# Performance work log

Hardware: AMD Instinct MI355X
Metric: run time of the kernel (lower is better)

The kernel has to match this reference:

```python
import jax, jax.numpy as jnp
import numpy as np

B, S, D, H = 4, 2048, 1024, 16
HD = D // H


def setup_inputs() -> dict:
    key = jax.random.key(0)
    ks = jax.random.split(key, 12)
    sc = 1.0 / np.sqrt(D)
    return {
        "x": jax.random.normal(ks[0], (B, S, D), dtype=jnp.float32),
        "key_padding_mask": jax.random.randint(ks[1], (B, S), 0, 2).astype(bool),
        "attn_mask_modifier": jax.random.uniform(ks[2], (B, S, S), dtype=jnp.float32),
        "Wq": jax.random.normal(ks[3], (D, D), dtype=jnp.float32) * sc,
        "bq": jax.random.normal(ks[4], (D,), dtype=jnp.float32) * sc,
        "Wk": jax.random.normal(ks[5], (D, D), dtype=jnp.float32) * sc,
        "bk": jax.random.normal(ks[6], (D,), dtype=jnp.float32) * sc,
        "Wv": jax.random.normal(ks[7], (D, D), dtype=jnp.float32) * sc,
        "bv": jax.random.normal(ks[8], (D,), dtype=jnp.float32) * sc,
        "Wo": jax.random.normal(ks[9], (D, D), dtype=jnp.float32) * sc,
        "bo": jax.random.normal(ks[10], (D,), dtype=jnp.float32) * sc,
    }


def reference(x, key_padding_mask, attn_mask_modifier, Wq, bq, Wk, bk, Wv, bv, Wo, bo):
    b, s, d = x.shape
    hd = d // H
    # QKV projections -> [b, H, s, hd]
    q = (x @ Wq + bq).reshape(b, s, H, hd).transpose(0, 2, 1, 3)
    k = (x @ Wk + bk).reshape(b, s, H, hd).transpose(0, 2, 1, 3)
    v = (x @ Wv + bv).reshape(b, s, H, hd).transpose(0, 2, 1, 3)
    energy = jnp.einsum("bhqd,bhkd->bhqk", q, k) / jnp.sqrt(jnp.asarray(hd, x.dtype))
    # handle_neg=False path: multiplicative mask modifier, broadcast over heads
    energy = energy * attn_mask_modifier[:, None, :, :]
    # key_padding_mask is applied on the QUERY axis (unsqueeze(1).unsqueeze(-1)) per source
    energy = jnp.where(key_padding_mask[:, None, :, None], jnp.asarray(-1e10, x.dtype), energy)
    attn = jax.nn.softmax(energy, axis=-1)
    out = jnp.einsum("bhqk,bhkd->bhqd", attn, v).transpose(0, 2, 1, 3).reshape(b, s, d)
    return out @ Wo + bo
```

## Files before the change

### kernel.cpp

```cpp
#include <hip/hip_runtime.h>
#include <cstddef>

constexpr int Bn  = 4;
constexpr int Sn  = 2048;
constexpr int Dn  = 1024;
constexpr int Hn  = 16;
constexpr int HDn = 64;

typedef __bf16 bf16;
typedef __attribute__((ext_vector_type(8))) __bf16 bf16x8;
typedef __attribute__((ext_vector_type(4))) __bf16 bf16x4;
typedef __attribute__((ext_vector_type(4))) float  f32x4;

typedef __attribute__((address_space(1))) const void gvoid;
typedef __attribute__((address_space(3))) void lvoid;

__global__ __launch_bounds__(256) void conv_f32_bf16_k(
    const float* __restrict__ in, bf16* __restrict__ out, int n)
{
    int i = (blockIdx.x * 256 + threadIdx.x) * 4;
    if (i + 3 < n) {
        float4 v = *(const float4*)(in + i);
        bf16 o[4] = {(bf16)v.x, (bf16)v.y, (bf16)v.z, (bf16)v.w};
        *(ulong1*)(out + i) = *(ulong1*)o;
    }
}

__global__ __launch_bounds__(256) void bias_cat_k(
    const float* __restrict__ bq, const float* __restrict__ bk,
    const float* __restrict__ bv, float* __restrict__ o)
{
    const int i = blockIdx.x * 256 + threadIdx.x;
    if (i < 1024)      o[i] = bq[i];
    else if (i < 2048) o[i] = bk[i - 1024];
    else if (i < 3072) o[i] = bv[i - 2048];
}

__global__ __launch_bounds__(256) void conv_wt_k(
    const float* __restrict__ w0, const float* __restrict__ w1,
    const float* __restrict__ w2, const float* __restrict__ w3,
    bf16* __restrict__ o0, bf16* __restrict__ o1,
    bf16* __restrict__ o2, bf16* __restrict__ o3)
{
    const float* W = (blockIdx.z == 0) ? w0 : (blockIdx.z == 1) ? w1
                   : (blockIdx.z == 2) ? w2 : w3;
    bf16* O = (blockIdx.z == 0) ? o0 : (blockIdx.z == 1) ? o1
            : (blockIdx.z == 2) ? o2 : o3;
    __shared__ float t[64][65];
    const int tid = threadIdx.x;
    const int k0 = blockIdx.x * 64;
    const int n0 = blockIdx.y * 64;
    #pragma unroll
    for (int p = 0; p < 16; ++p) {
        const int idx = p * 256 + tid;
        const int r = idx >> 6, c = idx & 63;
        t[r][c] = W[(size_t)(k0 + r) * Dn + n0 + c];
    }
    __syncthreads();
    #pragma unroll
    for (int p = 0; p < 16; ++p) {
        const int idx = p * 256 + tid;
        const int r = idx >> 6, c = idx & 63;
        O[(size_t)(n0 + r) * Dn + k0 + c] = (bf16)t[c][r];
    }
}

#define GEMM_STAGE(Ap, Bp, k0, boff)                                          \
    {                                                                         \
        _Pragma("unroll")                                                     \
        for (int j = 0; j < 4; ++j) {                                         \
            const int rbase = (w * 4 + j) * 8;                                \
            const int r = rbase + srow;                                       \
            __builtin_amdgcn_global_load_lds(                                 \
                (gvoid*)(Ap + (size_t)(m0 + r) * Dn + (k0) + scol),           \
                (lvoid*)&smem[(boff) + rbase * 64], 16, 0, 0);                \
            __builtin_amdgcn_global_load_lds(                                 \
                (gvoid*)(Bp + (size_t)(n0 + r) * Dn + (k0) + scol),           \
                (lvoid*)&smem[(boff) + 128 * 64 + rbase * 64], 16, 0, 0);     \
        }                                                                     \
    }

#define GEMM_COMPUTE(boff)                                                    \
    {                                                                         \
        _Pragma("unroll")                                                     \
        for (int ks = 0; ks < 64; ks += 32) {                                 \
            bf16x8 af[4], bfr[4];                                             \
            _Pragma("unroll")                                                 \
            for (int fm = 0; fm < 4; ++fm)                                    \
                af[fm] = *(const bf16x8*)&smem[(boff) +                       \
                    (wm * 64 + fm * 16 + l15) * 64 + ks + quad * 8];          \
            _Pragma("unroll")                                                 \
            for (int fn = 0; fn < 4; ++fn)                                    \
                bfr[fn] = *(const bf16x8*)&smem[(boff) + 128 * 64 +           \
                    (wn * 64 + fn * 16 + l15) * 64 + ks + quad * 8];          \
            _Pragma("unroll")                                                 \
            for (int fm = 0; fm < 4; ++fm)                                    \
                _Pragma("unroll")                                             \
                for (int fn = 0; fn < 4; ++fn)                                \
                    acc[fm][fn] = __builtin_amdgcn_mfma_f32_16x16x32_bf16(    \
                        af[fm], bfr[fn], acc[fm][fn], 0, 0, 0);               \
        }                                                                     \
    }

constexpr int BUF = 2 * 128 * 64;

__global__ __launch_bounds__(256) void gemm_out_k(
    const bf16* __restrict__ A, const bf16* __restrict__ Bt,
    const float* __restrict__ bias, float* __restrict__ outv)
{
    __shared__ __align__(16) bf16 smem[2 * BUF];

    const int tid  = threadIdx.x;
    const int w    = tid >> 6;
    const int lane = tid & 63;
    const int quad = lane >> 4;
    const int l15  = lane & 15;
    const int m0   = blockIdx.x * 128;
    const int n0   = blockIdx.y * 128;
    const int wm   = w >> 1;
    const int wn   = w & 1;
    const int srow = lane >> 3;
    const int scol = (lane & 7) * 8;

    f32x4 acc[4][4] = {};

    GEMM_STAGE(A, Bt, 0, 0);
    __syncthreads();

    int boff = 0;
    for (int kt = 0; kt < Dn / 64; ++kt) {
        if (kt + 1 < Dn / 64) GEMM_STAGE(A, Bt, (kt + 1) * 64, boff ^ BUF);
        GEMM_COMPUTE(boff);
        __syncthreads();
        boff ^= BUF;
    }

    #pragma unroll
    for (int fn = 0; fn < 4; ++fn) {
        const int c = n0 + wn * 64 + fn * 16 + l15;
        const float bv = bias[c];
        #pragma unroll
        for (int fm = 0; fm < 4; ++fm)
            #pragma unroll
            for (int i = 0; i < 4; ++i) {
                const int m = m0 + wm * 64 + fm * 16 + quad * 4 + i;
                outv[(size_t)m * Dn + c] = acc[fm][fn][i] + bv;
            }
    }
}

__global__ __launch_bounds__(256) void gemm_qkv_k(
    const bf16* __restrict__ A, const bf16* __restrict__ Wt,
    const float* __restrict__ bias, bf16* __restrict__ qout,
    bf16* __restrict__ kout, bf16* __restrict__ vout, float scq)
{
    __shared__ __align__(16) bf16 smem[2 * BUF];

    const int tid  = threadIdx.x;
    const int w    = tid >> 6;
    const int lane = tid & 63;
    const int quad = lane >> 4;
    const int l15  = lane & 15;
    const int m0   = blockIdx.x * 128;
    const int n0   = blockIdx.y * 128;
    const int wm   = w >> 1;
    const int wn   = w & 1;
    const int srow = lane >> 3;
    const int scol = (lane & 7) * 8;

    f32x4 acc[4][4] = {};

    GEMM_STAGE(A, Wt, 0, 0);
    __syncthreads();

    int boff = 0;
    for (int kt = 0; kt < Dn / 64; ++kt) {
        if (kt + 1 < Dn / 64) GEMM_STAGE(A, Wt, (kt + 1) * 64, boff ^ BUF);
        GEMM_COMPUTE(boff);
        __syncthreads();
        boff ^= BUF;
    }

    const int sec = n0 >> 10;
    const int cb  = n0 & 1023;

    if (sec < 2) {
        bf16* const outp = sec ? kout : qout;
        const float scale = sec ? 1.0f : scq;
        #pragma unroll
        for (int fn = 0; fn < 4; ++fn) {
            const int cc = cb + wn * 64 + fn * 16 + l15;
            const float bv = bias[n0 + wn * 64 + fn * 16 + l15];
            const int h = cc >> 6, hd = cc & 63;
            #pragma unroll
            for (int fm = 0; fm < 4; ++fm)
                #pragma unroll
                for (int i = 0; i < 4; ++i) {
                    const int m = m0 + wm * 64 + fm * 16 + quad * 4 + i;
                    const int b = m >> 11, s = m & (Sn - 1);
                    outp[(((size_t)(b * Hn + h) * Sn) + s) * HDn + hd] =
                        (bf16)((acc[fm][fn][i] + bv) * scale);
                }
        }
    } else {
        bf16* const T = smem;
        #pragma unroll
        for (int fn = 0; fn < 4; ++fn) {
            const int n = wn * 64 + fn * 16 + l15;
            const float bv = bias[n0 + n];
            #pragma unroll
            for (int fm = 0; fm < 4; ++fm) {
                const int m = wm * 64 + fm * 16 + quad * 4;
                bf16x4 pk;
                #pragma unroll
                for (int i = 0; i < 4; ++i)
                    pk[i] = (bf16)(acc[fm][fn][i] + bv);
                *(bf16x4*)&T[n * 136 + m] = pk;
            }
        }
        __syncthreads();
        const int b  = m0 >> 11;
        const int s0 = m0 & (Sn - 1);
        #pragma unroll
        for (int it = 0; it < 8; ++it) {
            const int n    = it * 16 + (tid >> 4);
            const int mcol = (tid & 15) * 8;
            const int gh = (cb + n) >> 6, ghd = (cb + n) & 63;
            bf16x8 v = *(const bf16x8*)&T[n * 136 + mcol];
            *(bf16x8*)(vout +
                (((size_t)(b * Hn + gh) * HDn) + ghd) * Sn + s0 + mcol) = v;
        }
    }
}

__device__ __forceinline__ int sidx(int r, int c) {
    return r * 64 + (c ^ ((r & 7) << 3));
}

__global__ __launch_bounds__(256) void attn_mfma_k(
    const bf16* __restrict__ Qb, const bf16* __restrict__ Kb,
    const bf16* __restrict__ Vtb, const int* __restrict__ kpm,
    const float* __restrict__ mod, bf16* __restrict__ att)
{
    __shared__ __align__(16) bf16 Ks[2][64 * 64];
    __shared__ __align__(16) bf16 Vts[2][64 * 64];
    __shared__ __align__(16) bf16 Ps[64 * 64];

    const int tid  = threadIdx.x;
    const int w    = tid >> 6;
    const int lane = tid & 63;
    const int quad = lane >> 4;
    const int l15  = lane & 15;
    const int blk  = blockIdx.x;
    const int bh   = blk >> 5;
    const int q0   = (blk & 31) * 64;
    const int b    = bh >> 4;
    const int h    = bh & 15;
    const size_t base = (size_t)bh * Sn * HDn;

    const int qrow = q0 + w * 16 + l15;
    const bf16x8 qf0 = *(const bf16x8*)(Qb + base + (size_t)qrow * HDn + 0  + quad * 8);
    const bf16x8 qf1 = *(const bf16x8*)(Qb + base + (size_t)qrow * HDn + 32 + quad * 8);

    const bool qm = kpm[(size_t)b * Sn + qrow] != 0;
    const float* modrow = mod + ((size_t)b * Sn + qrow) * Sn;

    float m_r = -1e30f;
    float l_r = 0.0f;
    f32x4 O[4] = {};

    const int rl = lane >> 3;
    const int cg = ((lane & 7) ^ rl) * 8;

    auto stage = [&](int t, int buf) {
        const int k0 = t * 64;
        #pragma unroll
        for (int p = 0; p < 2; ++p) {
            const int gb = p * 32 + w * 8;
            __builtin_amdgcn_global_load_lds(
                (gvoid*)(Kb + base + (size_t)(k0 + gb + rl) * HDn + cg),
                (lvoid*)&Ks[buf][gb * 64], 16, 0, 0);
            __builtin_amdgcn_global_load_lds(
                (gvoid*)(Vtb + base + (size_t)(gb + rl) * Sn + k0 + cg),
                (lvoid*)&Vts[buf][gb * 64], 16, 0, 0);
        }
    };

    stage(0, 0);
    float4 md[4];
    #pragma unroll
    for (int ct = 0; ct < 4; ++ct)
        md[ct] = *(const float4*)(modrow + ct * 16 + quad * 4);
    __syncthreads();

    constexpr int NT = Sn / 64;
    for (int t = 0; t < NT; ++t) {
        const int cur = t & 1;

        float4 mdn[4];
        if (t + 1 < NT) {
            stage(t + 1, cur ^ 1);
            #pragma unroll
            for (int ct = 0; ct < 4; ++ct)
                mdn[ct] = *(const float4*)(modrow + (t + 1) * 64 + ct * 16 + quad * 4);
        }

        float e[4][4];
        #pragma unroll
        for (int ct = 0; ct < 4; ++ct) {
            f32x4 s = {};
            #pragma unroll
            for (int ks = 0; ks < 64; ks += 32) {
                bf16x8 kf = *(const bf16x8*)&Ks[cur][sidx(ct * 16 + l15, ks + quad * 8)];
                s = __builtin_amdgcn_mfma_f32_16x16x32_bf16(kf, ks ? qf1 : qf0, s, 0, 0, 0);
            }
            #pragma unroll
            for (int i = 0; i < 4; ++i)
                e[ct][i] = qm ? -1e10f : s[i] * (&md[ct].x)[i];
        }

        float pmax = e[0][0];
        #pragma unroll
        for (int ct = 0; ct < 4; ++ct)
            #pragma unroll
            for (int i = 0; i < 4; ++i)
                pmax = fmaxf(pmax, e[ct][i]);
        pmax = fmaxf(pmax, __shfl_xor(pmax, 16));
        pmax = fmaxf(pmax, __shfl_xor(pmax, 32));

        if (__any(pmax > m_r + 8.0f)) {
            const float mnew  = fmaxf(m_r, pmax);
            const float alpha = __builtin_amdgcn_exp2f(m_r - mnew);
            m_r = mnew;
            l_r *= alpha;
            float aO[4];
            #pragma unroll
            for (int i = 0; i < 4; ++i)
                aO[i] = __shfl(alpha, quad * 4 + i, 16);
            #pragma unroll
            for (int ct = 0; ct < 4; ++ct)
                #pragma unroll
                for (int i = 0; i < 4; ++i)
                    O[ct][i] *= aO[i];
        }

        float rs = 0.0f;
        #pragma unroll
        for (int ct = 0; ct < 4; ++ct) {
            bf16x4 pb;
            #pragma unroll
            for (int i = 0; i < 4; ++i) {
                const bf16 p = (bf16)__builtin_amdgcn_exp2f(e[ct][i] - m_r);
                pb[i] = p;
                rs += (float)p;
            }
            *(bf16x4*)&Ps[sidx(w * 16 + l15, ct * 16 + quad * 4)] = pb;
        }
        rs += __shfl_xor(rs, 16);
        rs += __shfl_xor(rs, 32);
        l_r += rs;

        #pragma unroll
        for (int ks = 0; ks < 64; ks += 32) {
            bf16x8 paf = *(const bf16x8*)&Ps[sidx(w * 16 + l15, ks + quad * 8)];
            #pragma unroll
            for (int ct = 0; ct < 4; ++ct) {
                bf16x8 vf = *(const bf16x8*)&Vts[cur][sidx(ct * 16 + l15, ks + quad * 8)];
                O[ct] = __builtin_amdgcn_mfma_f32_16x16x32_bf16(paf, vf, O[ct], 0, 0, 0);
            }
        }

        if (t + 1 < NT) {
            #pragma unroll
            for (int ct = 0; ct < 4; ++ct)
                md[ct] = mdn[ct];
        }
        __syncthreads();
    }

    float lO[4];
    #pragma unroll
    for (int i = 0; i < 4; ++i)
        lO[i] = 1.0f / __shfl(l_r, quad * 4 + i, 16);
    #pragma unroll
    for (int ct = 0; ct < 4; ++ct)
        #pragma unroll
        for (int i = 0; i < 4; ++i) {
            const int row = q0 + w * 16 + quad * 4 + i;
            const int col = h * HDn + ct * 16 + l15;
            att[((size_t)b * Sn + row) * Dn + col] = (bf16)(O[ct][i] * lO[i]);
        }
}

extern "C" void kernel_launch(void* const* d_in, const int* in_sizes, int n_in,
                              void* d_out, int out_size, void* d_ws, size_t ws_size,
                              hipStream_t stream) {
    const float* x   = (const float*)d_in[0];
    const int*   kpm = (const int*)d_in[1];
    const float* mod = (const float*)d_in[2];
    const float* Wq  = (const float*)d_in[3];
    const float* bq  = (const float*)d_in[4];
    const float* Wk  = (const float*)d_in[5];
    const float* bk  = (const float*)d_in[6];
    const float* Wv  = (const float*)d_in[7];
    const float* bv  = (const float*)d_in[8];
    const float* Wo  = (const float*)d_in[9];
    const float* bo  = (const float*)d_in[10];
    float* out = (float*)d_out;

    bf16* ws = (bf16*)d_ws;
    const size_t sz = (size_t)Bn * Sn * Dn;
    const size_t wz = (size_t)Dn * Dn;
    bf16* xb   = ws;
    bf16* qb   = ws + sz;
    bf16* kb   = ws + 2 * sz;
    bf16* vtb  = ws + 3 * sz;
    bf16* attb = ws + 4 * sz;
    bf16* wqt  = ws + 5 * sz;
    bf16* wkt  = wqt + wz;
    bf16* wvt  = wkt + wz;
    bf16* wot  = wvt + wz;
    float* bqkv = (float*)(wot + wz);

    conv_f32_bf16_k<<<(int)(sz / 1024), 256, 0, stream>>>(x, xb, (int)sz);
    conv_wt_k<<<dim3(16, 16, 4), 256, 0, stream>>>(Wq, Wk, Wv, Wo, wqt, wkt, wvt, wot);
    bias_cat_k<<<12, 256, 0, stream>>>(bq, bk, bv, bqkv);

    const float SC = 0.125f * 1.44269504088896340736f;

    gemm_qkv_k<<<dim3(64, 24), 256, 0, stream>>>(xb, wqt, bqkv, qb, kb, vtb, SC);

    attn_mfma_k<<<Bn * Hn * (Sn / 64), 256, 0, stream>>>(qb, kb, vtb, kpm, mod, attb);

    gemm_out_k<<<dim3(64, 8), 256, 0, stream>>>(attb, wot, bo, out);
}
```

Baseline: 420.7 us.

## Double attention query tile to 128 rows and tighten GEMM pipeline sync

The attention kernel now uses 512-thread blocks covering 128 query rows. Each 64-row K/V tile is staged once per block and shared by 8 waves instead of 4, which halves K/V reload traffic and per-tile staging work per wave. The QKV and output GEMM k-loops replace __syncthreads with explicit vmcnt waits, raw barriers and sched_barriers so the next stage's loads can overlap compute. Smaller changes turn the query mask into an FMA bias and use tree-shaped max and sum reductions. Risks: lower occupancy from the larger blocks, the hard-coded vmcnt depending on the stage's load count, and the dominant per-head read of the mask modifier being unchanged.

```diff
diff --git a/kernel.cpp b/kernel.cpp
--- a/kernel.cpp
+++ b/kernel.cpp
@@ -102,6 +102,24 @@
         }                                                                     \
     }
 
+#define GEMM_KLOOP(Ap, Bp)                                                    \
+    GEMM_STAGE(Ap, Bp, 0, 0);                                                 \
+    int boff = 0;                                                             \
+    for (int kt = 0; kt < Dn / 64; ++kt) {                                    \
+        if (kt + 1 < Dn / 64) {                                               \
+            GEMM_STAGE(Ap, Bp, (kt + 1) * 64, boff ^ BUF);                    \
+            asm volatile("s_waitcnt vmcnt(8)" ::: "memory");                  \
+        } else {                                                              \
+            asm volatile("s_waitcnt vmcnt(0)" ::: "memory");                  \
+        }                                                                     \
+        __builtin_amdgcn_s_barrier();                                         \
+        __builtin_amdgcn_sched_barrier(0);                                    \
+        GEMM_COMPUTE(boff);                                                   \
+        __builtin_amdgcn_sched_barrier(0);                                    \
+        __builtin_amdgcn_s_barrier();                                         \
+        boff ^= BUF;                                                          \
+    }
+
 constexpr int BUF = 2 * 128 * 64;
 
 __global__ __launch_bounds__(256) void gemm_out_k(
@@ -124,16 +142,7 @@
 
     f32x4 acc[4][4] = {};
 
-    GEMM_STAGE(A, Bt, 0, 0);
-    __syncthreads();
-
-    int boff = 0;
-    for (int kt = 0; kt < Dn / 64; ++kt) {
-        if (kt + 1 < Dn / 64) GEMM_STAGE(A, Bt, (kt + 1) * 64, boff ^ BUF);
-        GEMM_COMPUTE(boff);
-        __syncthreads();
-        boff ^= BUF;
-    }
+    GEMM_KLOOP(A, Bt);
 
     #pragma unroll
     for (int fn = 0; fn < 4; ++fn) {
@@ -170,16 +179,7 @@
 
     f32x4 acc[4][4] = {};
 
-    GEMM_STAGE(A, Wt, 0, 0);
-    __syncthreads();
-
-    int boff = 0;
-    for (int kt = 0; kt < Dn / 64; ++kt) {
-        if (kt + 1 < Dn / 64) GEMM_STAGE(A, Wt, (kt + 1) * 64, boff ^ BUF);
-        GEMM_COMPUTE(boff);
-        __syncthreads();
-        boff ^= BUF;
-    }
+    GEMM_KLOOP(A, Wt);
 
     const int sec = n0 >> 10;
     const int cb  = n0 & 1023;
@@ -237,14 +237,14 @@
     return r * 64 + (c ^ ((r & 7) << 3));
 }
 
-__global__ __launch_bounds__(256) void attn_mfma_k(
+__global__ __launch_bounds__(512, 6) void attn_mfma_k(
     const bf16* __restrict__ Qb, const bf16* __restrict__ Kb,
     const bf16* __restrict__ Vtb, const int* __restrict__ kpm,
     const float* __restrict__ mod, bf16* __restrict__ att)
 {
     __shared__ __align__(16) bf16 Ks[2][64 * 64];
     __shared__ __align__(16) bf16 Vts[2][64 * 64];
-    __shared__ __align__(16) bf16 Ps[64 * 64];
+    __shared__ __align__(16) bf16 Ps[128 * 64];
 
     const int tid  = threadIdx.x;
     const int w    = tid >> 6;
@@ -252,8 +252,8 @@
     const int quad = lane >> 4;
     const int l15  = lane & 15;
     const int blk  = blockIdx.x;
-    const int bh   = blk >> 5;
-    const int q0   = (blk & 31) * 64;
+    const int bh   = blk >> 4;
+    const int q0   = (blk & 15) * 128;
     const int b    = bh >> 4;
     const int h    = bh & 15;
     const size_t base = (size_t)bh * Sn * HDn;
@@ -262,7 +262,7 @@
     const bf16x8 qf0 = *(const bf16x8*)(Qb + base + (size_t)qrow * HDn + 0  + quad * 8);
     const bf16x8 qf1 = *(const bf16x8*)(Qb + base + (size_t)qrow * HDn + 32 + quad * 8);
 
-    const bool qm = kpm[(size_t)b * Sn + qrow] != 0;
+    const float qbias = (kpm[(size_t)b * Sn + qrow] != 0) ? -1e30f : 0.0f;
     const float* modrow = mod + ((size_t)b * Sn + qrow) * Sn;
 
     float m_r = -1e30f;
@@ -271,19 +271,16 @@
 
     const int rl = lane >> 3;
     const int cg = ((lane & 7) ^ rl) * 8;
+    const int gb = w * 8;
 
     auto stage = [&](int t, int buf) {
         const int k0 = t * 64;
-        #pragma unroll
-        for (int p = 0; p < 2; ++p) {
-            const int gb = p * 32 + w * 8;
-            __builtin_amdgcn_global_load_lds(
-                (gvoid*)(Kb + base + (size_t)(k0 + gb + rl) * HDn + cg),
-                (lvoid*)&Ks[buf][gb * 64], 16, 0, 0);
-            __builtin_amdgcn_global_load_lds(
-                (gvoid*)(Vtb + base + (size_t)(gb + rl) * Sn + k0 + cg),
-                (lvoid*)&Vts[buf][gb * 64], 16, 0, 0);
-        }
+        __builtin_amdgcn_global_load_lds(
+            (gvoid*)(Kb + base + (size_t)(k0 + gb + rl) * HDn + cg),
+            (lvoid*)&Ks[buf][gb * 64], 16, 0, 0);
+        __builtin_amdgcn_global_load_lds(
+            (gvoid*)(Vtb + base + (size_t)(gb + rl) * Sn + k0 + cg),
+            (lvoid*)&Vts[buf][gb * 64], 16, 0, 0);
     };
 
     stage(0, 0);
@@ -316,15 +313,14 @@
             }
             #pragma unroll
             for (int i = 0; i < 4; ++i)
-                e[ct][i] = qm ? -1e10f : s[i] * (&md[ct].x)[i];
-        }
-
-        float pmax = e[0][0];
+                e[ct][i] = fmaf(s[i], (&md[ct].x)[i], qbias);
+        }
+
+        float pm[4];
         #pragma unroll
         for (int ct = 0; ct < 4; ++ct)
-            #pragma unroll
-            for (int i = 0; i < 4; ++i)
-                pmax = fmaxf(pmax, e[ct][i]);
+            pm[ct] = fmaxf(fmaxf(e[ct][0], e[ct][1]), fmaxf(e[ct][2], e[ct][3]));
+        float pmax = fmaxf(fmaxf(pm[0], pm[1]), fmaxf(pm[2], pm[3]));
         pmax = fmaxf(pmax, __shfl_xor(pmax, 16));
         pmax = fmaxf(pmax, __shfl_xor(pmax, 32));
 
@@ -344,18 +340,21 @@
                     O[ct][i] *= aO[i];
         }
 
-        float rs = 0.0f;
+        float rsc[4];
         #pragma unroll
         for (int ct = 0; ct < 4; ++ct) {
             bf16x4 pb;
+            float pf[4];
             #pragma unroll
             for (int i = 0; i < 4; ++i) {
                 const bf16 p = (bf16)__builtin_amdgcn_exp2f(e[ct][i] - m_r);
                 pb[i] = p;
-                rs += (float)p;
+                pf[i] = (float)p;
             }
+            rsc[ct] = (pf[0] + pf[1]) + (pf[2] + pf[3]);
             *(bf16x4*)&Ps[sidx(w * 16 + l15, ct * 16 + quad * 4)] = pb;
         }
+        float rs = (rsc[0] + rsc[1]) + (rsc[2] + rsc[3]);
         rs += __shfl_xor(rs, 16);
         rs += __shfl_xor(rs, 32);
         l_r += rs;
@@ -430,7 +429,7 @@
 
     gemm_qkv_k<<<dim3(64, 24), 256, 0, stream>>>(xb, wqt, bqkv, qb, kb, vtb, SC);
 
-    attn_mfma_k<<<Bn * Hn * (Sn / 64), 256, 0, stream>>>(qb, kb, vtb, kpm, mod, attb);
+    attn_mfma_k<<<Bn * Hn * (Sn / 128), 512, 0, stream>>>(qb, kb, vtb, kpm, mod, attb);
 
     gemm_out_k<<<dim3(64, 8), 256, 0, stream>>>(attb, wot, bo, out);
 }
```

Result: no change. 416.2 us (-1.1%).
